# Kernel tuning notes

Measured on AMD Instinct MI355X. Metric: run time of the kernel, lower is better.

## Reference

```python
import jax, jax.numpy as jnp
import numpy as np


def _unfold(x, k, stride, pad):
    """torch.nn.Unfold equivalent. x: [B,C,H,W] -> [B, C*k*k, L] with
    channel ordering (c, ki, kj) slow->fast and L = oh*ow row-major."""
    if pad:
        x = jnp.pad(x, ((0, 0), (0, 0), (pad, pad), (pad, pad)))
    B, C, H, W = x.shape
    oh = (H - k) // stride + 1
    ow = (W - k) // stride + 1
    r = jnp.arange(oh) * stride
    c = jnp.arange(ow) * stride
    xr = x[:, :, r[:, None] + jnp.arange(k)[None, :], :]          # [B,C,oh,k,W]
    xc = xr[:, :, :, :, c[:, None] + jnp.arange(k)[None, :]]      # [B,C,oh,ki,ow,kj]
    p = xc.transpose(0, 1, 3, 5, 2, 4)                            # [B,C,ki,kj,oh,ow]
    return p.reshape(B, C * k * k, oh * ow)


def _resize_bilinear(x, h, w):
    # matches F.interpolate(mode='bilinear', align_corners=False) for upsampling
    B, C = x.shape[0], x.shape[1]
    return jax.image.resize(x, (B, C, h, w), method='bilinear')


def setup_inputs() -> dict:
    key = jax.random.key(0)
    ks = jax.random.split(key, 8)
    bs, C, NC = 16, 768, 200
    x = jax.random.normal(ks[0], (bs, 784, C), jnp.float32)
    mask = jax.random.uniform(ks[1], (bs, 81), dtype=jnp.float32)
    img = jax.random.normal(ks[2], (bs, 3, 448, 448), jnp.float32)
    W_fc = jax.random.normal(ks[3], (NC, C), jnp.float32) * 0.02
    b_fc = jnp.zeros((NC,), jnp.float32)
    W_l = jax.random.normal(ks[4], (192, C), jnp.float32) * 0.02
    b_l = jnp.zeros((192,), jnp.float32)
    W_m = jax.random.normal(ks[5], (192, C), jnp.float32) * 0.02
    b_m = jnp.zeros((192,), jnp.float32)
    W_s = jax.random.normal(ks[6], (384, C), jnp.float32) * 0.02
    b_s = jnp.zeros((384,), jnp.float32)
    return dict(x=x, mask=mask, img=img, W_fc=W_fc, b_fc=b_fc,
                W_l=W_l, b_l=b_l, W_m=W_m, b_m=b_m, W_s=W_s, b_s=b_s)


def reference(x, mask, img, W_fc, b_fc, W_l, b_l, W_m, b_m, W_s, b_s):
    bs, C = x.shape[0], 768
    # im2col over image and feature map (all produce 81 = 9x9 windows)
    image_patches = _unfold(img, 128, 48, 32).transpose(0, 2, 1)   # [bs,81,3*128*128]
    feat = x.transpose(0, 2, 1).reshape(bs, C, 28, 28)
    patches_l = _unfold(feat, 8, 3, 2).transpose(0, 2, 1)          # [bs,81,C*64]
    patches_m = _unfold(feat, 6, 3, 1).transpose(0, 2, 1)          # [bs,81,C*36]
    patches_s = _unfold(feat, 4, 3, 0).transpose(0, 2, 1)          # [bs,81,C*16]
    # per-token class probabilities -> per-window importance score
    prob = jax.nn.softmax(x @ W_fc.T + b_fc, axis=-1)              # [bs,784,NC]
    max_logits = prob.max(axis=-1).reshape(bs, 1, 28, 28)
    part_logits = _unfold(max_logits, 8, 3, 2).mean(axis=1)        # [bs,81]
    part_logits = mask * part_logits
    sel = jnp.argmax(part_logits, axis=-1)                         # top-1 window id
    b_idx = jnp.arange(bs)
    parts_l = patches_l[b_idx, sel]                                # [bs,C*64]
    parts_m = patches_m[b_idx, sel]                                # [bs,C*36]
    parts_s = patches_s[b_idx, sel]                                # [bs,C*16]
    image_parts = image_patches[b_idx, sel]                        # [bs,3*128*128]
    # fold (single patch => reshape) + bilinear upsample to 8x8
    outl = parts_l.reshape(bs, C, 8, 8).transpose(0, 2, 3, 1).reshape(bs, 64, C)
    outm = _resize_bilinear(parts_m.reshape(bs, C, 6, 6), 8, 8)
    outm = outm.transpose(0, 2, 3, 1).reshape(bs, 64, C)
    outs = _resize_bilinear(parts_s.reshape(bs, C, 4, 4), 8, 8)
    outs = outs.transpose(0, 2, 3, 1).reshape(bs, 64, C)
    part1 = outl @ W_l.T + b_l                                     # [bs,64,192]
    part2 = outm @ W_m.T + b_m                                     # [bs,64,192]
    part3 = outs @ W_s.T + b_s                                     # [bs,64,384]
    ff_cat = jnp.concatenate([part1, part2, part3], axis=2)        # [bs,64,768]
    image_part = _resize_bilinear(image_parts.reshape(bs, 3, 128, 128), 224, 224)
    return ff_cat, image_part
```

## Files before the change

kernel.cpp:

```cpp
#include <hip/hip_runtime.h>
#include <math.h>

typedef __attribute__((ext_vector_type(8))) short bf16x8;
typedef __attribute__((ext_vector_type(4))) float f32x4;

__device__ __forceinline__ unsigned short f32_to_bf16_rne(float f) {
    unsigned int u = __float_as_uint(f);
    unsigned int r = (u + 0x7FFFu + ((u >> 16) & 1u)) >> 16;
    return (unsigned short)r;
}
__device__ __forceinline__ float bf16_to_f32(unsigned short h) {
    return __uint_as_float(((unsigned int)h) << 16);
}
__device__ __forceinline__ unsigned int pck(unsigned short a, unsigned short b) {
    return (unsigned int)a | ((unsigned int)b << 16);
}

__global__ __launch_bounds__(256) void k_prep(
    const float* __restrict__ Wfc, const float* __restrict__ Wl,
    const float* __restrict__ Wm, const float* __restrict__ Ws,
    unsigned short* __restrict__ Bpkh, unsigned short* __restrict__ Bpkl,
    unsigned short* __restrict__ B2h, unsigned short* __restrict__ B2l)
{
    const int blk = blockIdx.x, tid = threadIdx.x;
    const float* src; int idx, rows, cbase; bool isfc;
    if (blk < 192)      { isfc = true;  idx = blk * 256 + tid;        src = Wfc; rows = 200; cbase = 0; }
    else if (blk < 336) { isfc = false; idx = (blk - 192) * 256 + tid; src = Wl;  rows = 192; cbase = 0; }
    else if (blk < 480) { isfc = false; idx = (blk - 336) * 256 + tid; src = Wm;  rows = 192; cbase = 192; }
    else                { isfc = false; idx = (blk - 480) * 256 + tid; src = Ws;  rows = 384; cbase = 384; }
    const int c = idx / 192;
    const int kk = (idx % 192) * 4;
    unsigned short h[4] = {0, 0, 0, 0}, l[4] = {0, 0, 0, 0};
    if (c < rows) {
        const float4 w = *(const float4*)&src[(size_t)c * 768 + kk];
        const float wv[4] = {w.x, w.y, w.z, w.w};
#pragma unroll
        for (int j = 0; j < 4; ++j) {
            h[j] = f32_to_bf16_rne(wv[j]);
            l[j] = f32_to_bf16_rne(wv[j] - bf16_to_f32(h[j]));
        }
    }
    const int step = kk >> 5, oct = (kk & 31) >> 3, elem = kk & 7;
    const uint2 uh = make_uint2(pck(h[0], h[1]), pck(h[2], h[3]));
    const uint2 ul = make_uint2(pck(l[0], l[1]), pck(l[2], l[3]));
    if (isfc) {
        const size_t off = (size_t)((step * 16 + (c >> 4)) * 64 + oct * 16 + (c & 15)) * 8 + elem;
        *(uint2*)&Bpkh[off] = uh;
        *(uint2*)&Bpkl[off] = ul;
    } else {
        const int cg = cbase + c;
        const int tt = cg >> 6, cc = cg & 63;
        const size_t off = (size_t)(((tt * 24 + step) * 4 + (cc >> 4)) * 64 + oct * 16 + (cc & 15)) * 8 + elem;
        *(uint2*)&B2h[off] = uh;
        *(uint2*)&B2l[off] = ul;
    }
}

__global__ __launch_bounds__(256) void k_logits_fused(
    const float* __restrict__ x, const unsigned short* __restrict__ Bpkh,
    const unsigned short* __restrict__ Bpkl, const float* __restrict__ bfc,
    float* __restrict__ maxprob)
{
    __shared__ unsigned short AhS[2][4][64][8];
    __shared__ unsigned short AlS[2][4][64][8];
    __shared__ unsigned short BhS[2][16][64][8];
    __shared__ unsigned short BlS[2][16][64][8];
    __shared__ float sbias[256];
    __shared__ float red[4][64];
    __shared__ float red2[4][64];

    const int tid = threadIdx.x;
    const int lane = tid & 63;
    const int wid = tid >> 6;
    const int row0 = blockIdx.x * 64;

    sbias[tid] = (tid < 200) ? bfc[tid] : -1e30f;

    const int ar = tid & 63, ap = tid >> 6;
    const float* xb = x + (size_t)(row0 + ar) * 768 + ap * 8;
    const uint4* bhs = (const uint4*)Bpkh;
    const uint4* bls = (const uint4*)Bpkl;

    float ag[8];
    uint4 bgh[4], bgl[4];

    f32x4 acc[4][4];
    const f32x4 z = {0.f, 0.f, 0.f, 0.f};
#pragma unroll
    for (int mf = 0; mf < 4; ++mf)
#pragma unroll
        for (int q = 0; q < 4; ++q) acc[mf][q] = z;

    auto LOADAB = [&](int t) {
        const float4 v0 = *(const float4*)(xb + t * 32);
        const float4 v1 = *(const float4*)(xb + t * 32 + 4);
        ag[0] = v0.x; ag[1] = v0.y; ag[2] = v0.z; ag[3] = v0.w;
        ag[4] = v1.x; ag[5] = v1.y; ag[6] = v1.z; ag[7] = v1.w;
#pragma unroll
        for (int j = 0; j < 4; ++j) {
            bgh[j] = bhs[t * 1024 + j * 256 + tid];
            bgl[j] = bls[t * 1024 + j * 256 + tid];
        }
    };
    auto WRITEAB = [&](int buf) {
        unsigned short h[8], l[8];
#pragma unroll
        for (int j = 0; j < 8; ++j) {
            h[j] = f32_to_bf16_rne(ag[j]);
            l[j] = f32_to_bf16_rne(ag[j] - bf16_to_f32(h[j]));
        }
        *(uint4*)&AhS[buf][ar >> 4][ap * 16 + (ar & 15)][0] =
            make_uint4(pck(h[0], h[1]), pck(h[2], h[3]), pck(h[4], h[5]), pck(h[6], h[7]));
        *(uint4*)&AlS[buf][ar >> 4][ap * 16 + (ar & 15)][0] =
            make_uint4(pck(l[0], l[1]), pck(l[2], l[3]), pck(l[4], l[5]), pck(l[6], l[7]));
        uint4* bdh = (uint4*)&BhS[buf][0][0][0];
        uint4* bdl = (uint4*)&BlS[buf][0][0][0];
#pragma unroll
        for (int j = 0; j < 4; ++j) {
            bdh[j * 256 + tid] = bgh[j];
            bdl[j * 256 + tid] = bgl[j];
        }
    };

    LOADAB(0);
    WRITEAB(0);
    __syncthreads();

    for (int t = 0; t < 24; ++t) {
        const int cur = t & 1;
        if (t < 23) LOADAB(t + 1);
        bf16x8 ah[4], al2[4];
#pragma unroll
        for (int mf = 0; mf < 4; ++mf) {
            ah[mf]  = *(const bf16x8*)&AhS[cur][mf][lane][0];
            al2[mf] = *(const bf16x8*)&AlS[cur][mf][lane][0];
        }
#pragma unroll
        for (int q = 0; q < 4; ++q) {
            const bf16x8 bh = *(const bf16x8*)&BhS[cur][wid * 4 + q][lane][0];
            const bf16x8 bl = *(const bf16x8*)&BlS[cur][wid * 4 + q][lane][0];
#pragma unroll
            for (int mf = 0; mf < 4; ++mf) {
                acc[mf][q] = __builtin_amdgcn_mfma_f32_16x16x32_bf16(al2[mf], bh, acc[mf][q], 0, 0, 0);
                acc[mf][q] = __builtin_amdgcn_mfma_f32_16x16x32_bf16(ah[mf], bl, acc[mf][q], 0, 0, 0);
                acc[mf][q] = __builtin_amdgcn_mfma_f32_16x16x32_bf16(ah[mf], bh, acc[mf][q], 0, 0, 0);
            }
        }
        if (t < 23) WRITEAB(cur ^ 1);
        __syncthreads();
    }

    float bv[4];
#pragma unroll
    for (int q = 0; q < 4; ++q) bv[q] = sbias[wid * 64 + q * 16 + (lane & 15)];

    float mrow[4][4];
#pragma unroll
    for (int mf = 0; mf < 4; ++mf)
#pragma unroll
        for (int r = 0; r < 4; ++r) {
            float mx = -1e30f;
#pragma unroll
            for (int q = 0; q < 4; ++q) mx = fmaxf(mx, acc[mf][q][r] + bv[q]);
#pragma unroll
            for (int s = 1; s < 16; s <<= 1) mx = fmaxf(mx, __shfl_xor(mx, s, 64));
            mrow[mf][r] = mx;
            if ((lane & 15) == 0) red[wid][mf * 16 + (lane >> 4) * 4 + r] = mx;
        }
    __syncthreads();
#pragma unroll
    for (int mf = 0; mf < 4; ++mf)
#pragma unroll
        for (int r = 0; r < 4; ++r) {
            const int row = mf * 16 + (lane >> 4) * 4 + r;
            const float m = fmaxf(fmaxf(red[0][row], red[1][row]),
                                  fmaxf(red[2][row], red[3][row]));
            float se = 0.f;
#pragma unroll
            for (int q = 0; q < 4; ++q) se += __expf(acc[mf][q][r] + bv[q] - m);
#pragma unroll
            for (int s = 1; s < 16; s <<= 1) se += __shfl_xor(se, s, 64);
            if ((lane & 15) == 0) red2[wid][row] = se;
            (void)mrow[mf][r];
        }
    __syncthreads();
    if (wid == 0 && (lane & 15) == 0) {
#pragma unroll
        for (int mf = 0; mf < 4; ++mf)
#pragma unroll
            for (int r = 0; r < 4; ++r) {
                const int row = mf * 16 + (lane >> 4) * 4 + r;
                maxprob[row0 + row] = 1.0f /
                    (red2[0][row] + red2[1][row] + red2[2][row] + red2[3][row]);
            }
    }
}

__global__ void k_sel(const float* __restrict__ maxprob,
                      const float* __restrict__ mask, int* __restrict__ sel)
{
    __shared__ float mp[784];
    __shared__ float pl[81];
    const int b = blockIdx.x, tid = threadIdx.x;
    for (int i = tid; i < 784; i += blockDim.x) mp[i] = maxprob[b * 784 + i];
    __syncthreads();
    if (tid < 81) {
        const int pr = tid / 9, pc = tid % 9;
        float s = 0.f;
        for (int ki = 0; ki < 8; ++ki) {
            const int y = pr * 3 - 2 + ki;
            if (y < 0 || y >= 28) continue;
            for (int kj = 0; kj < 8; ++kj) {
                const int xx = pc * 3 - 2 + kj;
                if (xx < 0 || xx >= 28) continue;
                s += mp[y * 28 + xx];
            }
        }
        pl[tid] = mask[b * 81 + tid] * (s * (1.f / 64.f));
    }
    __syncthreads();
    if (tid == 0) {
        float best = pl[0]; int bi = 0;
        for (int i = 1; i < 81; ++i) if (pl[i] > best) { best = pl[i]; bi = i; }
        sel[b] = bi;
    }
}

__device__ __forceinline__ void rcoef8(int o, int n, int& f0, int& f1, float& w)
{
    float s = (o + 0.5f) * ((float)n * 0.125f) - 0.5f;
    s = fminf(fmaxf(s, 0.f), (float)(n - 1));
    f0 = (int)s;
    w = s - (float)f0;
    f1 = f0 + 1; if (f1 > n - 1) f1 = n - 1;
}

__global__ __launch_bounds__(256) void k_ff(
    const float* __restrict__ x, const int* __restrict__ sel,
    const unsigned short* __restrict__ B2h, const unsigned short* __restrict__ B2l,
    const float* __restrict__ bl, const float* __restrict__ bm,
    const float* __restrict__ bs_, float* __restrict__ out)
{
    __shared__ unsigned short AhS[2][4][64][8];
    __shared__ unsigned short AlS[2][4][64][8];
    __shared__ unsigned short BhS[2][4][64][8];
    __shared__ unsigned short BlS[2][4][64][8];

    const int blk = blockIdx.x;
    const int b = blk / 12, t = blk % 12;
    const int n0 = t * 64;
    const int seg = (t < 3) ? 0 : ((t < 6) ? 1 : 2);
    const float* bias = (seg == 0) ? (bl + t * 64)
                      : (seg == 1) ? (bm + (t - 3) * 64)
                                   : (bs_ + (t - 6) * 64);
    const int s = sel[b];
    const int wy0 = (s / 9) * 3 - 2, wx0 = (s % 9) * 3 - 2;

    const int tid = threadIdx.x;
    const int lane = tid & 63;
    const int wid = tid >> 6, wmi = wid & 1, wn = wid >> 1;

    const int gy = wy0 + (lane >> 3), gx = wx0 + (lane & 7);
    const bool inb = (gy >= 0 && gy < 28 && gx >= 0 && gx < 28);
    const float* xsrc = x + ((size_t)b * 784 + (inb ? (gy * 28 + gx) : 0)) * 768 + wid * 8;

    int r00, r01, r10, r11; float fx = 0.f, fy = 0.f;
    if (seg == 0) { r00 = r01 = r10 = r11 = lane; }
    else {
        const int nn = (seg == 1) ? 6 : 4, off = (seg == 1) ? 1 : 2;
        int f0y, f1y, f0x, f1x;
        rcoef8(lane >> 3, nn, f0y, f1y, fy);
        rcoef8(lane & 7, nn, f0x, f1x, fx);
        r00 = (off + f0y) * 8 + off + f0x;
        r01 = (off + f0y) * 8 + off + f1x;
        r10 = (off + f1y) * 8 + off + f0x;
        r11 = (off + f1y) * 8 + off + f1x;
    }

    const uint4* b2h = (const uint4*)B2h + (size_t)t * 24 * 256;
    const uint4* b2l = (const uint4*)B2l + (size_t)t * 24 * 256;

    float g[8];
    uint4 bh_r, bl_r;

    f32x4 acc[2][2];
    const f32x4 z = {0.f, 0.f, 0.f, 0.f};
#pragma unroll
    for (int mi = 0; mi < 2; ++mi)
#pragma unroll
        for (int q = 0; q < 2; ++q) acc[mi][q] = z;

    auto LOAD = [&](int st) {
        if (inb) {
            const float4 v0 = *(const float4*)(xsrc + st * 32);
            const float4 v1 = *(const float4*)(xsrc + st * 32 + 4);
            g[0] = v0.x; g[1] = v0.y; g[2] = v0.z; g[3] = v0.w;
            g[4] = v1.x; g[5] = v1.y; g[6] = v1.z; g[7] = v1.w;
        } else {
#pragma unroll
            for (int j = 0; j < 8; ++j) g[j] = 0.f;
        }
        bh_r = b2h[st * 256 + tid];
        bl_r = b2l[st * 256 + tid];
    };
    auto WRITE = [&](int buf) {
        unsigned short h[8], l[8];
#pragma unroll
        for (int j = 0; j < 8; ++j) {
            const float v00 = __shfl(g[j], r00, 64);
            const float v01 = __shfl(g[j], r01, 64);
            const float v10 = __shfl(g[j], r10, 64);
            const float v11 = __shfl(g[j], r11, 64);
            const float v0 = v00 + fx * (v01 - v00);
            const float v1 = v10 + fx * (v11 - v10);
            const float a = v0 + fy * (v1 - v0);
            h[j] = f32_to_bf16_rne(a);
            l[j] = f32_to_bf16_rne(a - bf16_to_f32(h[j]));
        }
        *(uint4*)&AhS[buf][lane >> 4][wid * 16 + (lane & 15)][0] =
            make_uint4(pck(h[0], h[1]), pck(h[2], h[3]), pck(h[4], h[5]), pck(h[6], h[7]));
        *(uint4*)&AlS[buf][lane >> 4][wid * 16 + (lane & 15)][0] =
            make_uint4(pck(l[0], l[1]), pck(l[2], l[3]), pck(l[4], l[5]), pck(l[6], l[7]));
        ((uint4*)&BhS[buf][0][0][0])[tid] = bh_r;
        ((uint4*)&BlS[buf][0][0][0])[tid] = bl_r;
    };

    LOAD(0);
    WRITE(0);
    __syncthreads();

    for (int st = 0; st < 24; ++st) {
        const int cur = st & 1;
        if (st < 23) LOAD(st + 1);
        bf16x8 ah[2], al2[2];
#pragma unroll
        for (int mi = 0; mi < 2; ++mi) {
            ah[mi]  = *(const bf16x8*)&AhS[cur][wmi * 2 + mi][lane][0];
            al2[mi] = *(const bf16x8*)&AlS[cur][wmi * 2 + mi][lane][0];
        }
#pragma unroll
        for (int q = 0; q < 2; ++q) {
            const bf16x8 bh = *(const bf16x8*)&BhS[cur][wn * 2 + q][lane][0];
            const bf16x8 bl2 = *(const bf16x8*)&BlS[cur][wn * 2 + q][lane][0];
#pragma unroll
            for (int mi = 0; mi < 2; ++mi) {
                acc[mi][q] = __builtin_amdgcn_mfma_f32_16x16x32_bf16(al2[mi], bh, acc[mi][q], 0, 0, 0);
                acc[mi][q] = __builtin_amdgcn_mfma_f32_16x16x32_bf16(ah[mi], bl2, acc[mi][q], 0, 0, 0);
                acc[mi][q] = __builtin_amdgcn_mfma_f32_16x16x32_bf16(ah[mi], bh, acc[mi][q], 0, 0, 0);
            }
        }
        if (st < 23) WRITE(cur ^ 1);
        __syncthreads();
    }

#pragma unroll
    for (int mi = 0; mi < 2; ++mi)
#pragma unroll
        for (int q = 0; q < 2; ++q)
#pragma unroll
            for (int r = 0; r < 4; ++r) {
                const int row = wmi * 32 + mi * 16 + (lane >> 4) * 4 + r;
                const int col = wn * 32 + q * 16 + (lane & 15);
                out[((size_t)b * 64 + row) * 768 + n0 + col] = acc[mi][q][r] + bias[col];
            }
}

__global__ __launch_bounds__(256) void k_image(
    const float* __restrict__ img, const int* __restrict__ sel,
    float* __restrict__ out)
{
    const int idx = blockIdx.x * 256 + threadIdx.x;
    if (idx >= 16 * 3 * 224 * 224) return;
    const int ox = idx % 224;
    int t = idx / 224;
    const int oy = t % 224; t /= 224;
    const int c = t % 3;
    const int b = t / 3;
    const int s = sel[b];
    const int ry0 = (s / 9) * 48 - 32, cx0 = (s % 9) * 48 - 32;

    float sy = (oy + 0.5f) * (128.f / 224.f) - 0.5f;
    sy = fminf(fmaxf(sy, 0.f), 127.f);
    const int fy0 = (int)sy; const float wy = sy - (float)fy0;
    const int fy1 = (fy0 < 127) ? fy0 + 1 : 127;

    float sx = (ox + 0.5f) * (128.f / 224.f) - 0.5f;
    sx = fminf(fmaxf(sx, 0.f), 127.f);
    const int fx0 = (int)sx; const float wx = sx - (float)fx0;
    const int fx1 = (fx0 < 127) ? fx0 + 1 : 127;

    const float* ib = img + ((size_t)b * 3 + c) * 448 * 448;
    auto rd = [&](int py, int px) -> float {
        const int r = ry0 + py, cc = cx0 + px;
        return (r >= 0 && r < 448 && cc >= 0 && cc < 448) ? ib[r * 448 + cc] : 0.f;
    };
    const float g00 = rd(fy0, fx0), g01 = rd(fy0, fx1);
    const float g10 = rd(fy1, fx0), g11 = rd(fy1, fx1);
    const float v0 = g00 + wx * (g01 - g00);
    const float v1 = g10 + wx * (g11 - g10);
    out[idx] = v0 + wy * (v1 - v0);
}

extern "C" void kernel_launch(void* const* d_in, const int* in_sizes, int n_in,
                              void* d_out, int out_size, void* d_ws, size_t ws_size,
                              hipStream_t stream)
{
    const float* x    = (const float*)d_in[0];
    const float* mask = (const float*)d_in[1];
    const float* img  = (const float*)d_in[2];
    const float* Wfc  = (const float*)d_in[3];
    const float* bfc  = (const float*)d_in[4];
    const float* Wl   = (const float*)d_in[5];
    const float* bl   = (const float*)d_in[6];
    const float* Wm   = (const float*)d_in[7];
    const float* bm   = (const float*)d_in[8];
    const float* Ws   = (const float*)d_in[9];
    const float* bs   = (const float*)d_in[10];
    float* out = (float*)d_out;

    char* ws = (char*)d_ws;
    float* maxprob       = (float*)ws;
    int*   sel           = (int*)(ws + 51200);
    unsigned short* Bpkh = (unsigned short*)(ws + 65536);
    unsigned short* Bpkl = (unsigned short*)(ws + 458752);
    unsigned short* B2h  = (unsigned short*)(ws + 851968);
    unsigned short* B2l  = (unsigned short*)(ws + 2031616);

    hipLaunchKernelGGL(k_prep,         dim3(768),  dim3(256), 0, stream,
                       Wfc, Wl, Wm, Ws, Bpkh, Bpkl, B2h, B2l);
    hipLaunchKernelGGL(k_logits_fused, dim3(196),  dim3(256), 0, stream,
                       x, Bpkh, Bpkl, bfc, maxprob);
    hipLaunchKernelGGL(k_sel,          dim3(16),   dim3(128), 0, stream,
                       maxprob, mask, sel);
    hipLaunchKernelGGL(k_ff,           dim3(192),  dim3(256), 0, stream,
                       x, sel, B2h, B2l, bl, bm, bs, out);
    hipLaunchKernelGGL(k_image,        dim3(9408), dim3(256), 0, stream,
                       img, sel, out + 786432);
}
```

Baseline: 226.5 us.

## Split logits GEMM across class halves and shrink tiles to raise block count

The logits kernel now uses 32-row tiles and splits the 256 padded classes into two halves via a second grid dimension. Each block writes a partial max and partial exp-sum, and k_sel merges the two halves with a log-sum-exp combine. The ff GEMM moves to 32-column tiles (384 blocks), with the packed weight layout changed to match, and both kernels drop LDS double buffering in favour of a single buffer with an extra barrier. The aim is to fill more of the MI355X's CUs with a small grid, at the cost of less reuse per block, more barriers and extra global traffic for the partial results.

```diff
diff --git a/kernel.cpp b/kernel.cpp
--- a/kernel.cpp
+++ b/kernel.cpp
@@ -24,7 +24,7 @@
 {
     const int blk = blockIdx.x, tid = threadIdx.x;
     const float* src; int idx, rows, cbase; bool isfc;
-    if (blk < 192)      { isfc = true;  idx = blk * 256 + tid;        src = Wfc; rows = 200; cbase = 0; }
+    if (blk < 192)      { isfc = true;  idx = blk * 256 + tid;         src = Wfc; rows = 200; cbase = 0; }
     else if (blk < 336) { isfc = false; idx = (blk - 192) * 256 + tid; src = Wl;  rows = 192; cbase = 0; }
     else if (blk < 480) { isfc = false; idx = (blk - 336) * 256 + tid; src = Wm;  rows = 192; cbase = 192; }
     else                { isfc = false; idx = (blk - 480) * 256 + tid; src = Ws;  rows = 384; cbase = 384; }
@@ -49,160 +49,164 @@
         *(uint2*)&Bpkl[off] = ul;
     } else {
         const int cg = cbase + c;
-        const int tt = cg >> 6, cc = cg & 63;
-        const size_t off = (size_t)(((tt * 24 + step) * 4 + (cc >> 4)) * 64 + oct * 16 + (cc & 15)) * 8 + elem;
+        const int tt = cg >> 5, cc = cg & 31;
+        const size_t off = (size_t)(((tt * 24 + step) * 2 + (cc >> 4)) * 64 + oct * 16 + (cc & 15)) * 8 + elem;
         *(uint2*)&B2h[off] = uh;
         *(uint2*)&B2l[off] = ul;
     }
 }
 
-__global__ __launch_bounds__(256) void k_logits_fused(
+__global__ __launch_bounds__(256) void k_logits_p(
     const float* __restrict__ x, const unsigned short* __restrict__ Bpkh,
     const unsigned short* __restrict__ Bpkl, const float* __restrict__ bfc,
-    float* __restrict__ maxprob)
-{
-    __shared__ unsigned short AhS[2][4][64][8];
-    __shared__ unsigned short AlS[2][4][64][8];
-    __shared__ unsigned short BhS[2][16][64][8];
-    __shared__ unsigned short BlS[2][16][64][8];
-    __shared__ float sbias[256];
-    __shared__ float red[4][64];
-    __shared__ float red2[4][64];
+    float* __restrict__ pmax, float* __restrict__ psum)
+{
+    __shared__ unsigned short Ah[2][64][8], Al[2][64][8];
+    __shared__ unsigned short Bh[8][64][8], Bl[8][64][8];
+    __shared__ float sbias[128];
+    __shared__ float red[4][32], red2[4][32];
 
     const int tid = threadIdx.x;
     const int lane = tid & 63;
     const int wid = tid >> 6;
-    const int row0 = blockIdx.x * 64;
-
-    sbias[tid] = (tid < 200) ? bfc[tid] : -1e30f;
-
-    const int ar = tid & 63, ap = tid >> 6;
-    const float* xb = x + (size_t)(row0 + ar) * 768 + ap * 8;
+    const int row0 = blockIdx.x * 32;
+    const int cb = blockIdx.y;
+
+    if (tid < 128) {
+        const int c = cb * 128 + tid;
+        sbias[tid] = (c < 200) ? bfc[c] : -1e30f;
+    }
+
+    const int ar = tid & 31, kq = tid >> 5;
+    const float* xb = x + (size_t)(row0 + ar) * 768 + kq * 4;
     const uint4* bhs = (const uint4*)Bpkh;
     const uint4* bls = (const uint4*)Bpkl;
 
-    float ag[8];
-    uint4 bgh[4], bgl[4];
-
-    f32x4 acc[4][4];
+    float ag[4];
+    uint4 bgh[2], bgl[2];
+
+    f32x4 acc[2][2];
     const f32x4 z = {0.f, 0.f, 0.f, 0.f};
 #pragma unroll
-    for (int mf = 0; mf < 4; ++mf)
-#pragma unroll
-        for (int q = 0; q < 4; ++q) acc[mf][q] = z;
+    for (int mf = 0; mf < 2; ++mf)
+#pragma unroll
+        for (int q = 0; q < 2; ++q) acc[mf][q] = z;
 
     auto LOADAB = [&](int t) {
-        const float4 v0 = *(const float4*)(xb + t * 32);
-        const float4 v1 = *(const float4*)(xb + t * 32 + 4);
-        ag[0] = v0.x; ag[1] = v0.y; ag[2] = v0.z; ag[3] = v0.w;
-        ag[4] = v1.x; ag[5] = v1.y; ag[6] = v1.z; ag[7] = v1.w;
+        const float4 v = *(const float4*)(xb + t * 32);
+        ag[0] = v.x; ag[1] = v.y; ag[2] = v.z; ag[3] = v.w;
+        const int base = t * 1024 + cb * 512;
+#pragma unroll
+        for (int j = 0; j < 2; ++j) {
+            bgh[j] = bhs[base + j * 256 + tid];
+            bgl[j] = bls[base + j * 256 + tid];
+        }
+    };
+    auto WRITEAB = [&]() {
+        unsigned short h[4], l[4];
 #pragma unroll
         for (int j = 0; j < 4; ++j) {
-            bgh[j] = bhs[t * 1024 + j * 256 + tid];
-            bgl[j] = bls[t * 1024 + j * 256 + tid];
-        }
-    };
-    auto WRITEAB = [&](int buf) {
-        unsigned short h[8], l[8];
-#pragma unroll
-        for (int j = 0; j < 8; ++j) {
             h[j] = f32_to_bf16_rne(ag[j]);
             l[j] = f32_to_bf16_rne(ag[j] - bf16_to_f32(h[j]));
         }
-        *(uint4*)&AhS[buf][ar >> 4][ap * 16 + (ar & 15)][0] =
-            make_uint4(pck(h[0], h[1]), pck(h[2], h[3]), pck(h[4], h[5]), pck(h[6], h[7]));
-        *(uint4*)&AlS[buf][ar >> 4][ap * 16 + (ar & 15)][0] =
-            make_uint4(pck(l[0], l[1]), pck(l[2], l[3]), pck(l[4], l[5]), pck(l[6], l[7]));
-        uint4* bdh = (uint4*)&BhS[buf][0][0][0];
-        uint4* bdl = (uint4*)&BlS[buf][0][0][0];
-#pragma unroll
-        for (int j = 0; j < 4; ++j) {
+        *(uint2*)&Ah[ar >> 4][(kq >> 1) * 16 + (ar & 15)][(kq & 1) * 4] =
+            make_uint2(pck(h[0], h[1]), pck(h[2], h[3]));
+        *(uint2*)&Al[ar >> 4][(kq >> 1) * 16 + (ar & 15)][(kq & 1) * 4] =
+            make_uint2(pck(l[0], l[1]), pck(l[2], l[3]));
+        uint4* bdh = (uint4*)&Bh[0][0][0];
+        uint4* bdl = (uint4*)&Bl[0][0][0];
+#pragma unroll
+        for (int j = 0; j < 2; ++j) {
             bdh[j * 256 + tid] = bgh[j];
             bdl[j * 256 + tid] = bgl[j];
         }
     };
 
     LOADAB(0);
-    WRITEAB(0);
+    WRITEAB();
     __syncthreads();
 
     for (int t = 0; t < 24; ++t) {
-        const int cur = t & 1;
         if (t < 23) LOADAB(t + 1);
-        bf16x8 ah[4], al2[4];
-#pragma unroll
-        for (int mf = 0; mf < 4; ++mf) {
-            ah[mf]  = *(const bf16x8*)&AhS[cur][mf][lane][0];
-            al2[mf] = *(const bf16x8*)&AlS[cur][mf][lane][0];
-        }
-#pragma unroll
-        for (int q = 0; q < 4; ++q) {
-            const bf16x8 bh = *(const bf16x8*)&BhS[cur][wid * 4 + q][lane][0];
-            const bf16x8 bl = *(const bf16x8*)&BlS[cur][wid * 4 + q][lane][0];
-#pragma unroll
-            for (int mf = 0; mf < 4; ++mf) {
+        bf16x8 ah[2], al2[2];
+#pragma unroll
+        for (int mf = 0; mf < 2; ++mf) {
+            ah[mf]  = *(const bf16x8*)&Ah[mf][lane][0];
+            al2[mf] = *(const bf16x8*)&Al[mf][lane][0];
+        }
+#pragma unroll
+        for (int q = 0; q < 2; ++q) {
+            const bf16x8 bh = *(const bf16x8*)&Bh[wid * 2 + q][lane][0];
+            const bf16x8 bl = *(const bf16x8*)&Bl[wid * 2 + q][lane][0];
+#pragma unroll
+            for (int mf = 0; mf < 2; ++mf) {
                 acc[mf][q] = __builtin_amdgcn_mfma_f32_16x16x32_bf16(al2[mf], bh, acc[mf][q], 0, 0, 0);
                 acc[mf][q] = __builtin_amdgcn_mfma_f32_16x16x32_bf16(ah[mf], bl, acc[mf][q], 0, 0, 0);
                 acc[mf][q] = __builtin_amdgcn_mfma_f32_16x16x32_bf16(ah[mf], bh, acc[mf][q], 0, 0, 0);
             }
         }
-        if (t < 23) WRITEAB(cur ^ 1);
         __syncthreads();
-    }
-
-    float bv[4];
-#pragma unroll
-    for (int q = 0; q < 4; ++q) bv[q] = sbias[wid * 64 + q * 16 + (lane & 15)];
-
-    float mrow[4][4];
-#pragma unroll
-    for (int mf = 0; mf < 4; ++mf)
+        if (t < 23) {
+            WRITEAB();
+            __syncthreads();
+        }
+    }
+
+    float bv[2];
+#pragma unroll
+    for (int q = 0; q < 2; ++q) bv[q] = sbias[wid * 32 + q * 16 + (lane & 15)];
+
+#pragma unroll
+    for (int mf = 0; mf < 2; ++mf)
 #pragma unroll
         for (int r = 0; r < 4; ++r) {
-            float mx = -1e30f;
-#pragma unroll
-            for (int q = 0; q < 4; ++q) mx = fmaxf(mx, acc[mf][q][r] + bv[q]);
+            float mx = fmaxf(acc[mf][0][r] + bv[0], acc[mf][1][r] + bv[1]);
 #pragma unroll
             for (int s = 1; s < 16; s <<= 1) mx = fmaxf(mx, __shfl_xor(mx, s, 64));
-            mrow[mf][r] = mx;
             if ((lane & 15) == 0) red[wid][mf * 16 + (lane >> 4) * 4 + r] = mx;
         }
     __syncthreads();
 #pragma unroll
-    for (int mf = 0; mf < 4; ++mf)
+    for (int mf = 0; mf < 2; ++mf)
 #pragma unroll
         for (int r = 0; r < 4; ++r) {
             const int row = mf * 16 + (lane >> 4) * 4 + r;
             const float m = fmaxf(fmaxf(red[0][row], red[1][row]),
                                   fmaxf(red[2][row], red[3][row]));
-            float se = 0.f;
-#pragma unroll
-            for (int q = 0; q < 4; ++q) se += __expf(acc[mf][q][r] + bv[q] - m);
+            float se = __expf(acc[mf][0][r] + bv[0] - m) + __expf(acc[mf][1][r] + bv[1] - m);
 #pragma unroll
             for (int s = 1; s < 16; s <<= 1) se += __shfl_xor(se, s, 64);
             if ((lane & 15) == 0) red2[wid][row] = se;
-            (void)mrow[mf][r];
         }
     __syncthreads();
     if (wid == 0 && (lane & 15) == 0) {
 #pragma unroll
-        for (int mf = 0; mf < 4; ++mf)
+        for (int mf = 0; mf < 2; ++mf)
 #pragma unroll
             for (int r = 0; r < 4; ++r) {
                 const int row = mf * 16 + (lane >> 4) * 4 + r;
-                maxprob[row0 + row] = 1.0f /
-                    (red2[0][row] + red2[1][row] + red2[2][row] + red2[3][row]);
+                const float m = fmaxf(fmaxf(red[0][row], red[1][row]),
+                                      fmaxf(red[2][row], red[3][row]));
+                pmax[(size_t)(row0 + row) * 2 + cb] = m;
+                psum[(size_t)(row0 + row) * 2 + cb] =
+                    red2[0][row] + red2[1][row] + red2[2][row] + red2[3][row];
             }
     }
 }
 
-__global__ void k_sel(const float* __restrict__ maxprob,
+__global__ void k_sel(const float* __restrict__ pmax, const float* __restrict__ psum,
                       const float* __restrict__ mask, int* __restrict__ sel)
 {
     __shared__ float mp[784];
     __shared__ float pl[81];
     const int b = blockIdx.x, tid = threadIdx.x;
-    for (int i = tid; i < 784; i += blockDim.x) mp[i] = maxprob[b * 784 + i];
+    for (int i = tid; i < 784; i += blockDim.x) {
+        const size_t row = (size_t)b * 784 + i;
+        const float m0 = pmax[row * 2], m1 = pmax[row * 2 + 1];
+        const float s0 = psum[row * 2], s1 = psum[row * 2 + 1];
+        const float M = fmaxf(m0, m1);
+        mp[i] = 1.0f / (s0 * __expf(m0 - M) + s1 * __expf(m1 - M));
+    }
     __syncthreads();
     if (tid < 81) {
         const int pr = tid / 9, pc = tid % 9;
@@ -241,24 +245,22 @@
     const float* __restrict__ bl, const float* __restrict__ bm,
     const float* __restrict__ bs_, float* __restrict__ out)
 {
-    __shared__ unsigned short AhS[2][4][64][8];
-    __shared__ unsigned short AlS[2][4][64][8];
-    __shared__ unsigned short BhS[2][4][64][8];
-    __shared__ unsigned short BlS[2][4][64][8];
+    __shared__ unsigned short AhS[4][64][8], AlS[4][64][8];
+    __shared__ unsigned short BhS[2][64][8], BlS[2][64][8];
 
     const int blk = blockIdx.x;
-    const int b = blk / 12, t = blk % 12;
-    const int n0 = t * 64;
-    const int seg = (t < 3) ? 0 : ((t < 6) ? 1 : 2);
-    const float* bias = (seg == 0) ? (bl + t * 64)
-                      : (seg == 1) ? (bm + (t - 3) * 64)
-                                   : (bs_ + (t - 6) * 64);
+    const int b = blk / 24, t = blk % 24;
+    const int n0 = t * 32;
+    const int seg = (t < 6) ? 0 : ((t < 12) ? 1 : 2);
+    const float* bias = (seg == 0) ? (bl + t * 32)
+                      : (seg == 1) ? (bm + (t - 6) * 32)
+                                   : (bs_ + (t - 12) * 32);
     const int s = sel[b];
     const int wy0 = (s / 9) * 3 - 2, wx0 = (s % 9) * 3 - 2;
 
     const int tid = threadIdx.x;
     const int lane = tid & 63;
-    const int wid = tid >> 6, wmi = wid & 1, wn = wid >> 1;
+    const int wid = tid >> 6;
 
     const int gy = wy0 + (lane >> 3), gx = wx0 + (lane & 7);
     const bool inb = (gy >= 0 && gy < 28 && gx >= 0 && gx < 28);
@@ -277,18 +279,15 @@
         r11 = (off + f1y) * 8 + off + f1x;
     }
 
-    const uint4* b2h = (const uint4*)B2h + (size_t)t * 24 * 256;
-    const uint4* b2l = (const uint4*)B2l + (size_t)t * 24 * 256;
+    const uint4* b2h = (const uint4*)B2h + (size_t)t * 24 * 128;
+    const uint4* b2l = (const uint4*)B2l + (size_t)t * 24 * 128;
 
     float g[8];
-    uint4 bh_r, bl_r;
-
-    f32x4 acc[2][2];
+    uint4 b_r;
+
+    f32x4 acc[2];
     const f32x4 z = {0.f, 0.f, 0.f, 0.f};
-#pragma unroll
-    for (int mi = 0; mi < 2; ++mi)
-#pragma unroll
-        for (int q = 0; q < 2; ++q) acc[mi][q] = z;
+    acc[0] = z; acc[1] = z;
 
     auto LOAD = [&](int st) {
         if (inb) {
@@ -300,10 +299,9 @@
 #pragma unroll
             for (int j = 0; j < 8; ++j) g[j] = 0.f;
         }
-        bh_r = b2h[st * 256 + tid];
-        bl_r = b2l[st * 256 + tid];
+        b_r = (tid < 128) ? b2h[st * 128 + tid] : b2l[st * 128 + (tid - 128)];
     };
-    auto WRITE = [&](int buf) {
+    auto WRITE = [&]() {
         unsigned short h[8], l[8];
 #pragma unroll
         for (int j = 0; j < 8; ++j) {
@@ -317,52 +315,45 @@
             h[j] = f32_to_bf16_rne(a);
             l[j] = f32_to_bf16_rne(a - bf16_to_f32(h[j]));
         }
-        *(uint4*)&AhS[buf][lane >> 4][wid * 16 + (lane & 15)][0] =
+        *(uint4*)&AhS[lane >> 4][wid * 16 + (lane & 15)][0] =
             make_uint4(pck(h[0], h[1]), pck(h[2], h[3]), pck(h[4], h[5]), pck(h[6], h[7]));
-        *(uint4*)&AlS[buf][lane >> 4][wid * 16 + (lane & 15)][0] =
+        *(uint4*)&AlS[lane >> 4][wid * 16 + (lane & 15)][0] =
             make_uint4(pck(l[0], l[1]), pck(l[2], l[3]), pck(l[4], l[5]), pck(l[6], l[7]));
-        ((uint4*)&BhS[buf][0][0][0])[tid] = bh_r;
-        ((uint4*)&BlS[buf][0][0][0])[tid] = bl_r;
+        if (tid < 128) ((uint4*)&BhS[0][0][0])[tid] = b_r;
+        else           ((uint4*)&BlS[0][0][0])[tid - 128] = b_r;
     };
 
     LOAD(0);
-    WRITE(0);
+    WRITE();
     __syncthreads();
 
     for (int st = 0; st < 24; ++st) {
-        const int cur = st & 1;
         if (st < 23) LOAD(st + 1);
-        bf16x8 ah[2], al2[2];
-#pragma unroll
-        for (int mi = 0; mi < 2; ++mi) {
-            ah[mi]  = *(const bf16x8*)&AhS[cur][wmi * 2 + mi][lane][0];
-            al2[mi] = *(const bf16x8*)&AlS[cur][wmi * 2 + mi][lane][0];
-        }
+        const bf16x8 ah = *(const bf16x8*)&AhS[wid][lane][0];
+        const bf16x8 al = *(const bf16x8*)&AlS[wid][lane][0];
 #pragma unroll
         for (int q = 0; q < 2; ++q) {
-            const bf16x8 bh = *(const bf16x8*)&BhS[cur][wn * 2 + q][lane][0];
-            const bf16x8 bl2 = *(const bf16x8*)&BlS[cur][wn * 2 + q][lane][0];
-#pragma unroll
-            for (int mi = 0; mi < 2; ++mi) {
-                acc[mi][q] = __builtin_amdgcn_mfma_f32_16x16x32_bf16(al2[mi], bh, acc[mi][q], 0, 0, 0);
-                acc[mi][q] = __builtin_amdgcn_mfma_f32_16x16x32_bf16(ah[mi], bl2, acc[mi][q], 0, 0, 0);
-                acc[mi][q] = __builtin_amdgcn_mfma_f32_16x16x32_bf16(ah[mi], bh, acc[mi][q], 0, 0, 0);
-            }
-        }
-        if (st < 23) WRITE(cur ^ 1);
+            const bf16x8 bh = *(const bf16x8*)&BhS[q][lane][0];
+            const bf16x8 blo = *(const bf16x8*)&BlS[q][lane][0];
+            acc[q] = __builtin_amdgcn_mfma_f32_16x16x32_bf16(al, bh, acc[q], 0, 0, 0);
+            acc[q] = __builtin_amdgcn_mfma_f32_16x16x32_bf16(ah, blo, acc[q], 0, 0, 0);
+            acc[q] = __builtin_amdgcn_mfma_f32_16x16x32_bf16(ah, bh, acc[q], 0, 0, 0);
+        }
         __syncthreads();
-    }
-
-#pragma unroll
-    for (int mi = 0; mi < 2; ++mi)
-#pragma unroll
-        for (int q = 0; q < 2; ++q)
-#pragma unroll
-            for (int r = 0; r < 4; ++r) {
-                const int row = wmi * 32 + mi * 16 + (lane >> 4) * 4 + r;
-                const int col = wn * 32 + q * 16 + (lane & 15);
-                out[((size_t)b * 64 + row) * 768 + n0 + col] = acc[mi][q][r] + bias[col];
-            }
+        if (st < 23) {
+            WRITE();
+            __syncthreads();
+        }
+    }
+
+#pragma unroll
+    for (int q = 0; q < 2; ++q)
+#pragma unroll
+        for (int r = 0; r < 4; ++r) {
+            const int row = wid * 16 + (lane >> 4) * 4 + r;
+            const int col = q * 16 + (lane & 15);
+            out[((size_t)b * 64 + row) * 768 + n0 + col] = acc[q][r] + bias[col];
+        }
 }
 
 __global__ __launch_bounds__(256) void k_image(
@@ -419,21 +410,22 @@
     float* out = (float*)d_out;
 
     char* ws = (char*)d_ws;
-    float* maxprob       = (float*)ws;
-    int*   sel           = (int*)(ws + 51200);
-    unsigned short* Bpkh = (unsigned short*)(ws + 65536);
-    unsigned short* Bpkl = (unsigned short*)(ws + 458752);
-    unsigned short* B2h  = (unsigned short*)(ws + 851968);
-    unsigned short* B2l  = (unsigned short*)(ws + 2031616);
-
-    hipLaunchKernelGGL(k_prep,         dim3(768),  dim3(256), 0, stream,
+    float* pmax          = (float*)ws;
+    float* psum          = (float*)(ws + 102400);
+    int*   sel           = (int*)(ws + 204800);
+    unsigned short* Bpkh = (unsigned short*)(ws + 262144);
+    unsigned short* Bpkl = (unsigned short*)(ws + 655360);
+    unsigned short* B2h  = (unsigned short*)(ws + 1048576);
+    unsigned short* B2l  = (unsigned short*)(ws + 2228224);
+
+    hipLaunchKernelGGL(k_prep,     dim3(768),    dim3(256), 0, stream,
                        Wfc, Wl, Wm, Ws, Bpkh, Bpkl, B2h, B2l);
-    hipLaunchKernelGGL(k_logits_fused, dim3(196),  dim3(256), 0, stream,
-                       x, Bpkh, Bpkl, bfc, maxprob);
-    hipLaunchKernelGGL(k_sel,          dim3(16),   dim3(128), 0, stream,
-                       maxprob, mask, sel);
-    hipLaunchKernelGGL(k_ff,           dim3(192),  dim3(256), 0, stream,
+    hipLaunchKernelGGL(k_logits_p, dim3(392, 2), dim3(256), 0, stream,
+                       x, Bpkh, Bpkl, bfc, pmax, psum);
+    hipLaunchKernelGGL(k_sel,      dim3(16),     dim3(128), 0, stream,
+                       pmax, psum, mask, sel);
+    hipLaunchKernelGGL(k_ff,       dim3(384),    dim3(256), 0, stream,
                        x, sel, B2h, B2l, bl, bm, bs, out);
-    hipLaunchKernelGGL(k_image,        dim3(9408), dim3(256), 0, stream,
+    hipLaunchKernelGGL(k_image,    dim3(9408),   dim3(256), 0, stream,
                        img, sel, out + 786432);
 }
```

After: 272.6 us. 20.4% more time.
